# Performance work log

Measured on AMD Instinct MI355X. Metric: run time of the kernel, lower is better.

The kernel has to match this reference:

```python
import jax, jax.numpy as jnp
import numpy as np

NUM_GRAPHS = 256  # static batch size (= batch_indices.max()+1 by construction)
EMBED = 32
HIDDEN = 256
DEPTH = 10


def setup_inputs() -> dict:
    key = jax.random.key(0)
    ks = jax.random.split(key, 16)
    N, M = 8192, 16384
    atom_features = jax.random.randint(ks[0], (N,), 0, 200, dtype=jnp.int32)
    bond_features = jax.random.randint(ks[1], (M,), 0, 10, dtype=jnp.int32)
    adjacency_matrix = jax.random.randint(ks[2], (N, N), 0, 2, dtype=jnp.int32)
    batch_indices = jnp.sort(jax.random.randint(ks[3], (N,), 0, NUM_GRAPHS, dtype=jnp.int32))
    s = 0.05
    atom_emb_table = jax.random.normal(ks[4], (200, EMBED), jnp.float32) * s
    bond_emb_table = jax.random.normal(ks[5], (10, EMBED), jnp.float32) * s
    msg_W = jax.random.normal(ks[6], (DEPTH, HIDDEN, 2 * EMBED), jnp.float32) * s
    msg_b = jax.random.normal(ks[7], (DEPTH, HIDDEN), jnp.float32) * s
    gru_Wih = jax.random.normal(ks[8], (DEPTH, 3 * EMBED, HIDDEN), jnp.float32) * s
    gru_Whh = jax.random.normal(ks[9], (DEPTH, 3 * EMBED, EMBED), jnp.float32) * s
    gru_bih = jax.random.normal(ks[10], (DEPTH, 3 * EMBED), jnp.float32) * s
    gru_bhh = jax.random.normal(ks[11], (DEPTH, 3 * EMBED), jnp.float32) * s
    pool_W = jax.random.normal(ks[12], (HIDDEN, EMBED), jnp.float32) * s
    pool_b = jax.random.normal(ks[13], (HIDDEN,), jnp.float32) * s
    return dict(atom_features=atom_features, bond_features=bond_features,
                adjacency_matrix=adjacency_matrix, batch_indices=batch_indices,
                atom_emb_table=atom_emb_table, bond_emb_table=bond_emb_table,
                msg_W=msg_W, msg_b=msg_b, gru_Wih=gru_Wih, gru_Whh=gru_Whh,
                gru_bih=gru_bih, gru_bhh=gru_bhh, pool_W=pool_W, pool_b=pool_b)


def _gru_step(x, h, Wih, Whh, bih, bhh):
    # single-step torch-style GRU cell: x [N,HIDDEN], h [N,EMBED]
    gi = x @ Wih.T + bih                      # [N, 3E]
    gh = h @ Whh.T + bhh                      # [N, 3E]
    i_r, i_z, i_n = jnp.split(gi, 3, axis=-1)
    h_r, h_z, h_n = jnp.split(gh, 3, axis=-1)
    r = jax.nn.sigmoid(i_r + h_r)
    z = jax.nn.sigmoid(i_z + h_z)
    n = jnp.tanh(i_n + r * h_n)
    return (1.0 - z) * n + z * h


def reference(atom_features, bond_features, adjacency_matrix, batch_indices,
              atom_emb_table, bond_emb_table, msg_W, msg_b,
              gru_Wih, gru_Whh, gru_bih, gru_bhh, pool_W, pool_b):
    h = atom_emb_table[atom_features]                      # [N, E]
    A = (adjacency_matrix != 0).astype(h.dtype)            # [N, N]
    deg = A.sum(axis=-1, keepdims=True)                    # [N, 1]
    inv_deg = 1.0 / jnp.maximum(deg, 1.0)
    has_nei = deg > 0
    for d in range(DEPTH):
        # mean over neighbors of Linear(concat(self, nei)) == affine in (self, mean_nei)
        nei_mean = (A @ h) * inv_deg                       # [N, E]
        W_self = msg_W[d][:, :EMBED]                       # [H, E]
        W_nei = msg_W[d][:, EMBED:]                        # [H, E]
        msg = h @ W_self.T + nei_mean @ W_nei.T + msg_b[d]  # [N, H]
        msg = jnp.where(has_nei, msg, 0.0)                 # zero message if no neighbors
        h = _gru_step(msg, h, gru_Wih[d], gru_Whh[d], gru_bih[d], gru_bhh[d])
        # dropout is identity in eval mode
    # segment-mean pooling over graphs (zeros for empty graphs)
    sums = jax.ops.segment_sum(h, batch_indices, num_segments=NUM_GRAPHS)      # [B, E]
    counts = jax.ops.segment_sum(jnp.ones((h.shape[0],), h.dtype), batch_indices,
                                 num_segments=NUM_GRAPHS)[:, None]             # [B, 1]
    graph_mean = jnp.where(counts > 0, sums / jnp.maximum(counts, 1.0), 0.0)
    graph_embeddings = graph_mean @ pool_W.T + pool_b                          # [B, H]
    bond_embeddings = bond_emb_table[bond_features]                            # [M, E]
    return h, bond_embeddings, graph_embeddings
```

## Files before the change

### kernel.cpp

```cpp
#include <hip/hip_runtime.h>
#include <stdint.h>

#define N_ATOMS 8192
#define EMBED   32
#define DEPTHN  10

typedef short bf16x8 __attribute__((ext_vector_type(8)));
typedef float f32x4  __attribute__((ext_vector_type(4)));

__device__ __forceinline__ unsigned short f2bf(float f){
    unsigned u = __builtin_bit_cast(unsigned, f);
    u = u + 0x7FFFu + ((u >> 16) & 1u);
    return (unsigned short)(u >> 16);
}

__global__ __launch_bounds__(256) void k_preA(const int* __restrict__ A,
                                              unsigned long long* __restrict__ mask,
                                              int row0)
{
    const int i = row0 + blockIdx.x;
    const int t = threadIdx.x, w = t >> 6, l = t & 63;
    const int* row = A + (size_t)i * N_ATOMS;
    __shared__ unsigned long long lm[128];
    #pragma unroll
    for (int k = 0; k < 32; ++k){
        int j = k*256 + t;
        unsigned long long m = __ballot(row[j] != 0);
        if (l == 0) lm[k*4 + w] = m;
    }
    __syncthreads();
    if (t < 128) mask[(size_t)i*128 + t] = lm[t];
}

__global__ __launch_bounds__(256) void k_pack(const unsigned* __restrict__ maskRM,
                                              unsigned* __restrict__ mP,
                                              float* __restrict__ deg,
                                              float* __restrict__ invdeg)
{
    const int grp = blockIdx.x, t = threadIdx.x;
    __shared__ unsigned lm[16*260];
    __shared__ int red[256];
    #pragma unroll
    for (int s = 0; s < 16; ++s)
        lm[s*260 + t] = maskRM[(size_t)grp*4096 + s*256 + t];
    __syncthreads();
    {
        int r = t >> 4, seg = t & 15, cnt = 0;
        #pragma unroll
        for (int k = 0; k < 16; ++k) cnt += __popc(lm[r*260 + seg*16 + k]);
        red[t] = cnt; __syncthreads();
        if (t < 16){
            int s = 0;
            #pragma unroll
            for (int k = 0; k < 16; ++k) s += red[t*16 + k];
            deg[grp*16 + t] = (float)s;
            invdeg[grp*16 + t] = 1.f / fmaxf((float)s, 1.f);
        }
    }
    unsigned* out = mP + (size_t)grp*4096;
    #pragma unroll
    for (int s = 0; s < 16; ++s){
        int W = s*256 + t;
        out[W] = lm[(W & 15)*260 + (W >> 4)];
    }
}

__global__ __launch_bounds__(256) void k_setup(
    const int* __restrict__ af, const float* __restrict__ atom_emb,
    const float* __restrict__ msgW, const float* __restrict__ msgb,
    const float* __restrict__ Wih, const float* __restrict__ bih,
    float* __restrict__ hA, unsigned short* __restrict__ hP,
    float* __restrict__ Wc, float* __restrict__ bc,
    const int* __restrict__ bfeat, const float* __restrict__ bondf,
    float* __restrict__ out1)
{
    const int blk = blockIdx.x, t = threadIdx.x;
    if (blk < 1024){
        int idx = blk*256 + t;
        int i = idx >> 5, e = idx & 31;
        float v = atom_emb[af[i]*EMBED + e];
        hA[idx] = v;
        int g = i >> 5, qd = (i >> 3) & 3, j8 = i & 7;
        hP[(size_t)((g*2 + (e>>4))*64 + qd*16 + (e&15))*8 + j8] = f2bf(v);
    } else if (blk < 1264){
        int o = (blk-1024)*256 + t;
        int d = o / 6144, r = o % 6144, g = r >> 6, e = r & 63;
        const float* wi = Wih  + (size_t)(d*96 + g)*256;
        const float* mw = msgW + (size_t)d*256*64 + e;
        float acc = 0.f;
        for (int hh = 0; hh < 256; ++hh) acc += wi[hh] * mw[hh*64];
        Wc[o] = acc;
    } else if (blk < 1268){
        int o = (blk-1264)*256 + t;
        if (o < 960){
            int d = o / 96;
            const float* wi = Wih + (size_t)o*256;
            const float* mb = msgb + d*256;
            float acc = 0.f;
            for (int hh = 0; hh < 256; ++hh) acc += wi[hh] * mb[hh];
            bc[o] = acc + bih[o];
        }
    } else {
        int idx = (blk-1268)*256 + t;
        out1[idx] = bondf[bfeat[idx >> 5]*EMBED + (idx & 31)];
    }
}

__global__ __launch_bounds__(256) void k_nei(const unsigned short* __restrict__ hP,
                                             const unsigned* __restrict__ mP,
                                             float* __restrict__ neipart)
{
    __shared__ uint2 lut[16];
    const int rb = blockIdx.x & 63;
    const int q  = blockIdx.x >> 6;
    const int t = threadIdx.x, w = t >> 6, lane = t & 63;
    if (t < 16){
        unsigned lo = ((t & 1) ? 0x3F80u : 0u) | ((t & 2) ? 0x3F800000u : 0u);
        unsigned hi = ((t & 4) ? 0x3F80u : 0u) | ((t & 8) ? 0x3F800000u : 0u);
        lut[t] = make_uint2(lo, hi);
    }
    __syncthreads();
    const int n = lane & 15, quad = lane >> 4;
    const int rt0 = rb*8 + w*2;

    f32x4 a00 = {0.f,0.f,0.f,0.f};
    f32x4 a01 = {0.f,0.f,0.f,0.f};
    f32x4 a10 = {0.f,0.f,0.f,0.f};
    f32x4 a11 = {0.f,0.f,0.f,0.f};

    const unsigned* m0 = mP + (size_t)rt0*4096 + n;
    const unsigned* m1 = m0 + 4096;
    #pragma unroll 4
    for (int kk = 0; kk < 32; ++kk){
        const int g = q*32 + kk;
        union { uint4 u; bf16x8 v; } b0, b1;
        b0.u = *(const uint4*)&hP[(size_t)((g*2+0)*64 + lane)*8];
        b1.u = *(const uint4*)&hP[(size_t)((g*2+1)*64 + lane)*8];
        unsigned by0 = (m0[g*16] >> (quad*8)) & 0xFFu;
        unsigned by1 = (m1[g*16] >> (quad*8)) & 0xFFu;
        union { uint2 d[2]; bf16x8 v; } af0, af1;
        af0.d[0] = lut[by0 & 15u];
        af0.d[1] = lut[by0 >> 4];
        af1.d[0] = lut[by1 & 15u];
        af1.d[1] = lut[by1 >> 4];
        a00 = __builtin_amdgcn_mfma_f32_16x16x32_bf16(af0.v, b0.v, a00, 0, 0, 0);
        a01 = __builtin_amdgcn_mfma_f32_16x16x32_bf16(af0.v, b1.v, a01, 0, 0, 0);
        a10 = __builtin_amdgcn_mfma_f32_16x16x32_bf16(af1.v, b0.v, a10, 0, 0, 0);
        a11 = __builtin_amdgcn_mfma_f32_16x16x32_bf16(af1.v, b1.v, a11, 0, 0, 0);
    }
    float* outp = neipart + (size_t)q * N_ATOMS * EMBED;
    #pragma unroll
    for (int r = 0; r < 4; ++r){
        int row0 = rt0*16 + quad*4 + r;
        int row1 = row0 + 16;
        outp[(size_t)row0*EMBED + n]      = a00[r];
        outp[(size_t)row0*EMBED + 16 + n] = a01[r];
        outp[(size_t)row1*EMBED + n]      = a10[r];
        outp[(size_t)row1*EMBED + 16 + n] = a11[r];
    }
}

__global__ __launch_bounds__(256) void k_gru(
    const float* __restrict__ hin, float* __restrict__ hout,
    const float* __restrict__ neipart,
    const float* __restrict__ invdeg, const float* __restrict__ deg,
    const float* __restrict__ Wc, const float* __restrict__ bc,
    const float* __restrict__ bihf, const float* __restrict__ bhhf,
    const float* __restrict__ Whhf,
    unsigned short* __restrict__ hP, float* __restrict__ out0, int last)
{
    __shared__ float xs[16][68];
    const int t = threadIdx.x, blk = blockIdx.x;
    if (t < 128){
        float4 v = *(const float4*)&hin[(size_t)blk*512 + t*4];
        int a = t >> 3, e = (t*4) & 31;
        *(float4*)&xs[a][e] = v;
    } else {
        int u = t - 128;
        int a = u >> 3, e = (u*4) & 31;
        float4 s = {0.f,0.f,0.f,0.f};
        #pragma unroll
        for (int q = 0; q < 8; ++q){
            float4 v2 = *(const float4*)&neipart[(size_t)q*N_ATOMS*EMBED + blk*512 + u*4];
            s.x += v2.x; s.y += v2.y; s.z += v2.z; s.w += v2.w;
        }
        *(float4*)&xs[a][32 + e] = s;
    }
    __syncthreads();

    const int a = t & 15, p = t >> 4;
    const int atom = blk*16 + a;
    const float idg = invdeg[atom];
    const bool nz = deg[atom] > 0.f;
    float x[64];
    #pragma unroll
    for (int r = 0; r < 16; ++r){
        float4 v = *(const float4*)&xs[a][r*4];
        x[r*4+0]=v.x; x[r*4+1]=v.y; x[r*4+2]=v.z; x[r*4+3]=v.w;
    }
    #pragma unroll
    for (int e = 32; e < 64; ++e) x[e] *= idg;

    const int g = atom >> 5, qd = (atom >> 3) & 3, j8 = atom & 7;
    #pragma unroll
    for (int jj = 0; jj < 2; ++jj){
        const int j = p*2 + jj;
        const float* wr = Wc + j*64;
        const float* wz = Wc + (32+j)*64;
        const float* wn = Wc + (64+j)*64;
        float gr=0.f, gz=0.f, gn=0.f;
        #pragma unroll
        for (int e = 0; e < 64; ++e){ gr += wr[e]*x[e]; gz += wz[e]*x[e]; gn += wn[e]*x[e]; }
        if (nz){ gr += bc[j]; gz += bc[32+j]; gn += bc[64+j]; }
        else   { gr  = bihf[j]; gz = bihf[32+j]; gn = bihf[64+j]; }
        const float* vr = Whhf + j*32;
        const float* vz = Whhf + (32+j)*32;
        const float* vn = Whhf + (64+j)*32;
        float hr=bhhf[j], hz=bhhf[32+j], hn=bhhf[64+j];
        #pragma unroll
        for (int e = 0; e < 32; ++e){ hr += vr[e]*x[e]; hz += vz[e]*x[e]; hn += vn[e]*x[e]; }
        float rg = 1.f/(1.f + expf(-(gr+hr)));
        float zg = 1.f/(1.f + expf(-(gz+hz)));
        float ng = tanhf(gn + rg*hn);
        float hnew = (1.f - zg)*ng + zg*x[j];
        hout[(size_t)atom*EMBED + j] = hnew;
        hP[(size_t)((g*2 + (j>>4))*64 + qd*16 + (j&15))*8 + j8] = f2bf(hnew);
        if (last) out0[(size_t)atom*EMBED + j] = hnew;
    }
}

__global__ __launch_bounds__(256) void k_pool(
    const float* __restrict__ h, const int* __restrict__ batch,
    const float* __restrict__ poolW, const float* __restrict__ poolb,
    float* __restrict__ out2)
{
    const int b = blockIdx.x, t = threadIdx.x;
    int lo, hi;
    { int l = 0, r = N_ATOMS; while (l < r){ int m = (l+r)>>1; if (batch[m] < b)   l = m+1; else r = m; } lo = l; }
    { int l = 0, r = N_ATOMS; while (l < r){ int m = (l+r)>>1; if (batch[m] < b+1) l = m+1; else r = m; } hi = l; }
    const int cnt = hi - lo;
    __shared__ float ps[8][32];
    __shared__ float mean[32];
    const int e = t & 31, g = t >> 5;
    float acc = 0.f;
    for (int a = lo + g; a < hi; a += 8) acc += h[(size_t)a*EMBED + e];
    ps[g][e] = acc; __syncthreads();
    if (t < 32){
        float s = 0.f;
        #pragma unroll
        for (int gg = 0; gg < 8; ++gg) s += ps[gg][t];
        mean[t] = (cnt > 0) ? s / (float)cnt : 0.f;
    }
    __syncthreads();
    float emb = poolb[t];
    #pragma unroll
    for (int ee = 0; ee < 32; ++ee) emb += mean[ee] * poolW[t*32 + ee];
    out2[b*256 + t] = emb;
}

extern "C" void kernel_launch(void* const* d_in, const int* in_sizes, int n_in,
                              void* d_out, int out_size, void* d_ws, size_t ws_size,
                              hipStream_t stream)
{
    (void)in_sizes; (void)n_in; (void)out_size;
    const int* af   = (const int*)d_in[0];
    const int* bfe  = (const int*)d_in[1];
    const int* A    = (const int*)d_in[2];
    const int* bidx = (const int*)d_in[3];
    const float* atom_emb = (const float*)d_in[4];
    const float* bond_emb = (const float*)d_in[5];
    const float* msgW  = (const float*)d_in[6];
    const float* msgb  = (const float*)d_in[7];
    const float* Wih   = (const float*)d_in[8];
    const float* Whh   = (const float*)d_in[9];
    const float* bih   = (const float*)d_in[10];
    const float* bhh   = (const float*)d_in[11];
    const float* poolW = (const float*)d_in[12];
    const float* poolb = (const float*)d_in[13];

    float* out0 = (float*)d_out;
    float* out1 = out0 + 262144;
    float* out2 = out1 + 524288;

    float* deg    = out2;
    float* invdeg = out2 + 8192;

    unsigned long long* maskRM;
    unsigned*       mP;
    float*          hA; float* hB; float* Wc; float* bc; float* neipart;
    unsigned short* hP;
    const int wsok = (ws_size >= (size_t)33554432) ? 1 : 0;
    if (wsok){
        char* W = (char*)d_ws;
        maskRM  = (unsigned long long*)(W + 0);
        mP      = (unsigned*)(W + 8388608);
        hP      = (unsigned short*)(W + 16777216);
        hA      = (float*)(W + 17825792);
        hB      = (float*)(W + 18874368);
        Wc      = (float*)(W + 19922944);
        bc      = (float*)(W + 20185088);
        neipart = (float*)(W + 20971520);
        k_preA<<<dim3(8192), dim3(256), 0, stream>>>(A, maskRM, 0);
    } else {
        char* Ab = (char*)d_in[2];
        hA      = (float*)(Ab + 0);
        hB      = (float*)(Ab + 1048576);
        hP      = (unsigned short*)(Ab + 2097152);
        Wc      = (float*)(Ab + 2621440);
        bc      = (float*)(Ab + 2867200);
        neipart = (float*)(Ab + 4194304);
        mP      = (unsigned*)(Ab + 13631488);
        maskRM  = (unsigned long long*)(Ab + 260046848);
        k_preA<<<dim3(1),    dim3(256), 0, stream>>>(A, maskRM, 8191);
        k_preA<<<dim3(7),    dim3(256), 0, stream>>>(A, maskRM, 8184);
        k_preA<<<dim3(248),  dim3(256), 0, stream>>>(A, maskRM, 7936);
        k_preA<<<dim3(7936), dim3(256), 0, stream>>>(A, maskRM, 0);
    }
    k_pack<<<dim3(512), dim3(256), 0, stream>>>((const unsigned*)maskRM, mP,
        deg, invdeg);
    k_setup<<<dim3(3316), dim3(256), 0, stream>>>(af, atom_emb, msgW, msgb,
        Wih, bih, hA, hP, Wc, bc, bfe, bond_emb, out1);

    float* hin = hA; float* hout = hB;
    for (int d = 0; d < DEPTHN; ++d){
        k_nei<<<dim3(512), dim3(256), 0, stream>>>(hP, mP, neipart);
        k_gru<<<dim3(512), dim3(256), 0, stream>>>(hin, hout, neipart, invdeg, deg,
            Wc + d*6144, bc + d*96, bih + d*96, bhh + d*96, Whh + d*3072,
            hP, out0, (d == DEPTHN-1) ? 1 : 0);
        float* tmp = hin; hin = hout; hout = tmp;
    }
    k_pool<<<dim3(256), dim3(256), 0, stream>>>(hin, bidx, poolW, poolb, out2);
}
```

Baseline: 727.8 us.

## Fuse neighbor aggregation and GRU into one per-depth kernel with ping-pong bf16 buffers

Merges the neighbor-sum MFMA kernel and the GRU kernel into a single 512-thread kernel per depth. Each block now covers 32 atoms, and its 8 waves split the K dimension and reduce partial sums through shared memory instead of a global neipart buffer. The packed bf16 h buffer is double-buffered so one depth can read the old state while writing the new one. The pack and setup kernels are also merged into one launch. This removes global round-trips and half the launches, but only 256 blocks run per depth, which may limit parallelism.

```diff
diff --git a/kernel.cpp b/kernel.cpp
--- a/kernel.cpp
+++ b/kernel.cpp
@@ -32,40 +32,9 @@
     if (t < 128) mask[(size_t)i*128 + t] = lm[t];
 }
 
-__global__ __launch_bounds__(256) void k_pack(const unsigned* __restrict__ maskRM,
-                                              unsigned* __restrict__ mP,
-                                              float* __restrict__ deg,
-                                              float* __restrict__ invdeg)
-{
-    const int grp = blockIdx.x, t = threadIdx.x;
-    __shared__ unsigned lm[16*260];
-    __shared__ int red[256];
-    #pragma unroll
-    for (int s = 0; s < 16; ++s)
-        lm[s*260 + t] = maskRM[(size_t)grp*4096 + s*256 + t];
-    __syncthreads();
-    {
-        int r = t >> 4, seg = t & 15, cnt = 0;
-        #pragma unroll
-        for (int k = 0; k < 16; ++k) cnt += __popc(lm[r*260 + seg*16 + k]);
-        red[t] = cnt; __syncthreads();
-        if (t < 16){
-            int s = 0;
-            #pragma unroll
-            for (int k = 0; k < 16; ++k) s += red[t*16 + k];
-            deg[grp*16 + t] = (float)s;
-            invdeg[grp*16 + t] = 1.f / fmaxf((float)s, 1.f);
-        }
-    }
-    unsigned* out = mP + (size_t)grp*4096;
-    #pragma unroll
-    for (int s = 0; s < 16; ++s){
-        int W = s*256 + t;
-        out[W] = lm[(W & 15)*260 + (W >> 4)];
-    }
-}
-
-__global__ __launch_bounds__(256) void k_setup(
+__global__ __launch_bounds__(256) void k_prep(
+    const unsigned* __restrict__ maskRM, unsigned* __restrict__ mP,
+    float* __restrict__ deg, float* __restrict__ invdeg,
     const int* __restrict__ af, const float* __restrict__ atom_emb,
     const float* __restrict__ msgW, const float* __restrict__ msgb,
     const float* __restrict__ Wih, const float* __restrict__ bih,
@@ -74,158 +43,180 @@
     const int* __restrict__ bfeat, const float* __restrict__ bondf,
     float* __restrict__ out1)
 {
-    const int blk = blockIdx.x, t = threadIdx.x;
-    if (blk < 1024){
-        int idx = blk*256 + t;
-        int i = idx >> 5, e = idx & 31;
-        float v = atom_emb[af[i]*EMBED + e];
-        hA[idx] = v;
-        int g = i >> 5, qd = (i >> 3) & 3, j8 = i & 7;
-        hP[(size_t)((g*2 + (e>>4))*64 + qd*16 + (e&15))*8 + j8] = f2bf(v);
-    } else if (blk < 1264){
-        int o = (blk-1024)*256 + t;
-        int d = o / 6144, r = o % 6144, g = r >> 6, e = r & 63;
-        const float* wi = Wih  + (size_t)(d*96 + g)*256;
-        const float* mw = msgW + (size_t)d*256*64 + e;
-        float acc = 0.f;
-        for (int hh = 0; hh < 256; ++hh) acc += wi[hh] * mw[hh*64];
-        Wc[o] = acc;
-    } else if (blk < 1268){
-        int o = (blk-1264)*256 + t;
-        if (o < 960){
-            int d = o / 96;
-            const float* wi = Wih + (size_t)o*256;
-            const float* mb = msgb + d*256;
+    const int t = threadIdx.x;
+    if (blockIdx.x < 512){
+        const int grp = blockIdx.x;
+        __shared__ unsigned lm[16*260];
+        __shared__ int red[256];
+        #pragma unroll
+        for (int s = 0; s < 16; ++s)
+            lm[s*260 + t] = maskRM[(size_t)grp*4096 + s*256 + t];
+        __syncthreads();
+        {
+            int r = t >> 4, seg = t & 15, cnt = 0;
+            #pragma unroll
+            for (int k = 0; k < 16; ++k) cnt += __popc(lm[r*260 + seg*16 + k]);
+            red[t] = cnt; __syncthreads();
+            if (t < 16){
+                int s = 0;
+                #pragma unroll
+                for (int k = 0; k < 16; ++k) s += red[t*16 + k];
+                deg[grp*16 + t] = (float)s;
+                invdeg[grp*16 + t] = 1.f / fmaxf((float)s, 1.f);
+            }
+        }
+        unsigned* out = mP + (size_t)grp*4096;
+        #pragma unroll
+        for (int s = 0; s < 16; ++s){
+            int W = s*256 + t;
+            out[W] = lm[(W & 15)*260 + (W >> 4)];
+        }
+    } else {
+        const int blk = blockIdx.x - 512;
+        if (blk < 1024){
+            int idx = blk*256 + t;
+            int i = idx >> 5, e = idx & 31;
+            float v = atom_emb[af[i]*EMBED + e];
+            hA[idx] = v;
+            int g = i >> 5, qd = (i >> 3) & 3, j8 = i & 7;
+            hP[(size_t)((g*2 + (e>>4))*64 + qd*16 + (e&15))*8 + j8] = f2bf(v);
+        } else if (blk < 1264){
+            int o = (blk-1024)*256 + t;
+            int d = o / 6144, r = o % 6144, g = r >> 6, e = r & 63;
+            const float* wi = Wih  + (size_t)(d*96 + g)*256;
+            const float* mw = msgW + (size_t)d*256*64 + e;
             float acc = 0.f;
-            for (int hh = 0; hh < 256; ++hh) acc += wi[hh] * mb[hh];
-            bc[o] = acc + bih[o];
-        }
-    } else {
-        int idx = (blk-1268)*256 + t;
-        out1[idx] = bondf[bfeat[idx >> 5]*EMBED + (idx & 31)];
-    }
-}
-
-__global__ __launch_bounds__(256) void k_nei(const unsigned short* __restrict__ hP,
-                                             const unsigned* __restrict__ mP,
-                                             float* __restrict__ neipart)
+            for (int hh = 0; hh < 256; ++hh) acc += wi[hh] * mw[hh*64];
+            Wc[o] = acc;
+        } else if (blk < 1268){
+            int o = (blk-1264)*256 + t;
+            if (o < 960){
+                int d = o / 96;
+                const float* wi = Wih + (size_t)o*256;
+                const float* mb = msgb + d*256;
+                float acc = 0.f;
+                for (int hh = 0; hh < 256; ++hh) acc += wi[hh] * mb[hh];
+                bc[o] = acc + bih[o];
+            }
+        } else {
+            int idx = (blk-1268)*256 + t;
+            out1[idx] = bondf[bfeat[idx >> 5]*EMBED + (idx & 31)];
+        }
+    }
+}
+
+__global__ __launch_bounds__(512) void k_depth(
+    const unsigned short* __restrict__ hPin,
+    const unsigned* __restrict__ mP,
+    const float* __restrict__ hin, float* __restrict__ hout,
+    const float* __restrict__ invdeg, const float* __restrict__ deg,
+    const float* __restrict__ Wc, const float* __restrict__ bc,
+    const float* __restrict__ bihf, const float* __restrict__ bhhf,
+    const float* __restrict__ Whhf,
+    unsigned short* __restrict__ hPout, float* __restrict__ out0, int last)
 {
     __shared__ uint2 lut[16];
-    const int rb = blockIdx.x & 63;
-    const int q  = blockIdx.x >> 6;
-    const int t = threadIdx.x, w = t >> 6, lane = t & 63;
+    __shared__ float part[8][32][33];
+    __shared__ float xs[32][68];
+    const int t = threadIdx.x, blk = blockIdx.x;
     if (t < 16){
         unsigned lo = ((t & 1) ? 0x3F80u : 0u) | ((t & 2) ? 0x3F800000u : 0u);
         unsigned hi = ((t & 4) ? 0x3F80u : 0u) | ((t & 8) ? 0x3F800000u : 0u);
         lut[t] = make_uint2(lo, hi);
     }
     __syncthreads();
-    const int n = lane & 15, quad = lane >> 4;
-    const int rt0 = rb*8 + w*2;
-
-    f32x4 a00 = {0.f,0.f,0.f,0.f};
-    f32x4 a01 = {0.f,0.f,0.f,0.f};
-    f32x4 a10 = {0.f,0.f,0.f,0.f};
-    f32x4 a11 = {0.f,0.f,0.f,0.f};
-
-    const unsigned* m0 = mP + (size_t)rt0*4096 + n;
-    const unsigned* m1 = m0 + 4096;
-    #pragma unroll 4
-    for (int kk = 0; kk < 32; ++kk){
-        const int g = q*32 + kk;
-        union { uint4 u; bf16x8 v; } b0, b1;
-        b0.u = *(const uint4*)&hP[(size_t)((g*2+0)*64 + lane)*8];
-        b1.u = *(const uint4*)&hP[(size_t)((g*2+1)*64 + lane)*8];
-        unsigned by0 = (m0[g*16] >> (quad*8)) & 0xFFu;
-        unsigned by1 = (m1[g*16] >> (quad*8)) & 0xFFu;
-        union { uint2 d[2]; bf16x8 v; } af0, af1;
-        af0.d[0] = lut[by0 & 15u];
-        af0.d[1] = lut[by0 >> 4];
-        af1.d[0] = lut[by1 & 15u];
-        af1.d[1] = lut[by1 >> 4];
-        a00 = __builtin_amdgcn_mfma_f32_16x16x32_bf16(af0.v, b0.v, a00, 0, 0, 0);
-        a01 = __builtin_amdgcn_mfma_f32_16x16x32_bf16(af0.v, b1.v, a01, 0, 0, 0);
-        a10 = __builtin_amdgcn_mfma_f32_16x16x32_bf16(af1.v, b0.v, a10, 0, 0, 0);
-        a11 = __builtin_amdgcn_mfma_f32_16x16x32_bf16(af1.v, b1.v, a11, 0, 0, 0);
-    }
-    float* outp = neipart + (size_t)q * N_ATOMS * EMBED;
-    #pragma unroll
-    for (int r = 0; r < 4; ++r){
-        int row0 = rt0*16 + quad*4 + r;
-        int row1 = row0 + 16;
-        outp[(size_t)row0*EMBED + n]      = a00[r];
-        outp[(size_t)row0*EMBED + 16 + n] = a01[r];
-        outp[(size_t)row1*EMBED + n]      = a10[r];
-        outp[(size_t)row1*EMBED + 16 + n] = a11[r];
-    }
-}
-
-__global__ __launch_bounds__(256) void k_gru(
-    const float* __restrict__ hin, float* __restrict__ hout,
-    const float* __restrict__ neipart,
-    const float* __restrict__ invdeg, const float* __restrict__ deg,
-    const float* __restrict__ Wc, const float* __restrict__ bc,
-    const float* __restrict__ bihf, const float* __restrict__ bhhf,
-    const float* __restrict__ Whhf,
-    unsigned short* __restrict__ hP, float* __restrict__ out0, int last)
-{
-    __shared__ float xs[16][68];
-    const int t = threadIdx.x, blk = blockIdx.x;
-    if (t < 128){
-        float4 v = *(const float4*)&hin[(size_t)blk*512 + t*4];
-        int a = t >> 3, e = (t*4) & 31;
-        *(float4*)&xs[a][e] = v;
-    } else {
-        int u = t - 128;
-        int a = u >> 3, e = (u*4) & 31;
-        float4 s = {0.f,0.f,0.f,0.f};
-        #pragma unroll
-        for (int q = 0; q < 8; ++q){
-            float4 v2 = *(const float4*)&neipart[(size_t)q*N_ATOMS*EMBED + blk*512 + u*4];
-            s.x += v2.x; s.y += v2.y; s.z += v2.z; s.w += v2.w;
-        }
-        *(float4*)&xs[a][32 + e] = s;
-    }
-    __syncthreads();
-
-    const int a = t & 15, p = t >> 4;
-    const int atom = blk*16 + a;
-    const float idg = invdeg[atom];
-    const bool nz = deg[atom] > 0.f;
-    float x[64];
-    #pragma unroll
-    for (int r = 0; r < 16; ++r){
-        float4 v = *(const float4*)&xs[a][r*4];
-        x[r*4+0]=v.x; x[r*4+1]=v.y; x[r*4+2]=v.z; x[r*4+3]=v.w;
-    }
-    #pragma unroll
-    for (int e = 32; e < 64; ++e) x[e] *= idg;
-
-    const int g = atom >> 5, qd = (atom >> 3) & 3, j8 = atom & 7;
-    #pragma unroll
-    for (int jj = 0; jj < 2; ++jj){
-        const int j = p*2 + jj;
-        const float* wr = Wc + j*64;
-        const float* wz = Wc + (32+j)*64;
-        const float* wn = Wc + (64+j)*64;
-        float gr=0.f, gz=0.f, gn=0.f;
-        #pragma unroll
-        for (int e = 0; e < 64; ++e){ gr += wr[e]*x[e]; gz += wz[e]*x[e]; gn += wn[e]*x[e]; }
-        if (nz){ gr += bc[j]; gz += bc[32+j]; gn += bc[64+j]; }
-        else   { gr  = bihf[j]; gz = bihf[32+j]; gn = bihf[64+j]; }
-        const float* vr = Whhf + j*32;
-        const float* vz = Whhf + (32+j)*32;
-        const float* vn = Whhf + (64+j)*32;
-        float hr=bhhf[j], hz=bhhf[32+j], hn=bhhf[64+j];
-        #pragma unroll
-        for (int e = 0; e < 32; ++e){ hr += vr[e]*x[e]; hz += vz[e]*x[e]; hn += vn[e]*x[e]; }
-        float rg = 1.f/(1.f + expf(-(gr+hr)));
-        float zg = 1.f/(1.f + expf(-(gz+hz)));
-        float ng = tanhf(gn + rg*hn);
-        float hnew = (1.f - zg)*ng + zg*x[j];
-        hout[(size_t)atom*EMBED + j] = hnew;
-        hP[(size_t)((g*2 + (j>>4))*64 + qd*16 + (j&15))*8 + j8] = f2bf(hnew);
-        if (last) out0[(size_t)atom*EMBED + j] = hnew;
+    {
+        const int q = t >> 6, lane = t & 63;
+        const int n = lane & 15, quad = lane >> 4;
+        const int rt0 = blk*2;
+        f32x4 a00 = {0.f,0.f,0.f,0.f};
+        f32x4 a01 = {0.f,0.f,0.f,0.f};
+        f32x4 a10 = {0.f,0.f,0.f,0.f};
+        f32x4 a11 = {0.f,0.f,0.f,0.f};
+        const unsigned* m0 = mP + (size_t)rt0*4096 + n;
+        const unsigned* m1 = m0 + 4096;
+        #pragma unroll 4
+        for (int kk = 0; kk < 32; ++kk){
+            const int g = q*32 + kk;
+            union { uint4 u; bf16x8 v; } b0, b1;
+            b0.u = *(const uint4*)&hPin[(size_t)((g*2+0)*64 + lane)*8];
+            b1.u = *(const uint4*)&hPin[(size_t)((g*2+1)*64 + lane)*8];
+            unsigned by0 = (m0[g*16] >> (quad*8)) & 0xFFu;
+            unsigned by1 = (m1[g*16] >> (quad*8)) & 0xFFu;
+            union { uint2 d[2]; bf16x8 v; } af0, af1;
+            af0.d[0] = lut[by0 & 15u];
+            af0.d[1] = lut[by0 >> 4];
+            af1.d[0] = lut[by1 & 15u];
+            af1.d[1] = lut[by1 >> 4];
+            a00 = __builtin_amdgcn_mfma_f32_16x16x32_bf16(af0.v, b0.v, a00, 0, 0, 0);
+            a01 = __builtin_amdgcn_mfma_f32_16x16x32_bf16(af0.v, b1.v, a01, 0, 0, 0);
+            a10 = __builtin_amdgcn_mfma_f32_16x16x32_bf16(af1.v, b0.v, a10, 0, 0, 0);
+            a11 = __builtin_amdgcn_mfma_f32_16x16x32_bf16(af1.v, b1.v, a11, 0, 0, 0);
+        }
+        #pragma unroll
+        for (int r = 0; r < 4; ++r){
+            int rl = quad*4 + r;
+            part[q][rl][n]       = a00[r];
+            part[q][rl][16+n]    = a01[r];
+            part[q][16+rl][n]    = a10[r];
+            part[q][16+rl][16+n] = a11[r];
+        }
+    }
+    __syncthreads();
+    {
+        #pragma unroll
+        for (int ii = 0; ii < 2; ++ii){
+            int i = ii*512 + t;
+            int a = i >> 5, e = i & 31;
+            float s = 0.f;
+            #pragma unroll
+            for (int q = 0; q < 8; ++q) s += part[q][a][e];
+            xs[a][32+e] = s;
+            xs[a][e] = hin[(size_t)blk*1024 + i];
+        }
+    }
+    __syncthreads();
+    {
+        const int a = t & 15, pw = t >> 4;
+        const int al = a + (pw & 16);
+        const int p  = pw & 15;
+        const int atom = blk*32 + al;
+        const float idg = invdeg[atom];
+        const bool nz = deg[atom] > 0.f;
+        float x[64];
+        #pragma unroll
+        for (int r = 0; r < 16; ++r){
+            float4 v = *(const float4*)&xs[al][r*4];
+            x[r*4+0]=v.x; x[r*4+1]=v.y; x[r*4+2]=v.z; x[r*4+3]=v.w;
+        }
+        #pragma unroll
+        for (int e = 32; e < 64; ++e) x[e] *= idg;
+        const int gg = atom >> 5, qd = (atom >> 3) & 3, j8 = atom & 7;
+        #pragma unroll
+        for (int jj = 0; jj < 2; ++jj){
+            const int j = p*2 + jj;
+            const float* wr = Wc + j*64;
+            const float* wz = Wc + (32+j)*64;
+            const float* wn = Wc + (64+j)*64;
+            float gr=0.f, gz=0.f, gn=0.f;
+            #pragma unroll
+            for (int e = 0; e < 64; ++e){ gr += wr[e]*x[e]; gz += wz[e]*x[e]; gn += wn[e]*x[e]; }
+            if (nz){ gr += bc[j]; gz += bc[32+j]; gn += bc[64+j]; }
+            else   { gr  = bihf[j]; gz = bihf[32+j]; gn = bihf[64+j]; }
+            const float* vr = Whhf + j*32;
+            const float* vz = Whhf + (32+j)*32;
+            const float* vn = Whhf + (64+j)*32;
+            float hr=bhhf[j], hz=bhhf[32+j], hn=bhhf[64+j];
+            #pragma unroll
+            for (int e = 0; e < 32; ++e){ hr += vr[e]*x[e]; hz += vz[e]*x[e]; hn += vn[e]*x[e]; }
+            float rg = 1.f/(1.f + expf(-(gr+hr)));
+            float zg = 1.f/(1.f + expf(-(gz+hz)));
+            float ng = tanhf(gn + rg*hn);
+            float hnew = (1.f - zg)*ng + zg*x[j];
+            hout[(size_t)atom*EMBED + j] = hnew;
+            hPout[(size_t)((gg*2 + (j>>4))*64 + qd*16 + (j&15))*8 + j8] = f2bf(hnew);
+            if (last) out0[(size_t)atom*EMBED + j] = hnew;
+        }
     }
 }
 
@@ -287,28 +278,28 @@
 
     unsigned long long* maskRM;
     unsigned*       mP;
-    float*          hA; float* hB; float* Wc; float* bc; float* neipart;
-    unsigned short* hP;
+    float*          hA; float* hB; float* Wc; float* bc;
+    unsigned short* hP0; unsigned short* hP1;
     const int wsok = (ws_size >= (size_t)33554432) ? 1 : 0;
     if (wsok){
         char* W = (char*)d_ws;
         maskRM  = (unsigned long long*)(W + 0);
         mP      = (unsigned*)(W + 8388608);
-        hP      = (unsigned short*)(W + 16777216);
+        hP0     = (unsigned short*)(W + 16777216);
         hA      = (float*)(W + 17825792);
         hB      = (float*)(W + 18874368);
         Wc      = (float*)(W + 19922944);
         bc      = (float*)(W + 20185088);
-        neipart = (float*)(W + 20971520);
+        hP1     = (unsigned short*)(W + 20971520);
         k_preA<<<dim3(8192), dim3(256), 0, stream>>>(A, maskRM, 0);
     } else {
         char* Ab = (char*)d_in[2];
         hA      = (float*)(Ab + 0);
         hB      = (float*)(Ab + 1048576);
-        hP      = (unsigned short*)(Ab + 2097152);
+        hP0     = (unsigned short*)(Ab + 2097152);
         Wc      = (float*)(Ab + 2621440);
         bc      = (float*)(Ab + 2867200);
-        neipart = (float*)(Ab + 4194304);
+        hP1     = (unsigned short*)(Ab + 4194304);
         mP      = (unsigned*)(Ab + 13631488);
         maskRM  = (unsigned long long*)(Ab + 260046848);
         k_preA<<<dim3(1),    dim3(256), 0, stream>>>(A, maskRM, 8191);
@@ -316,18 +307,18 @@
         k_preA<<<dim3(248),  dim3(256), 0, stream>>>(A, maskRM, 7936);
         k_preA<<<dim3(7936), dim3(256), 0, stream>>>(A, maskRM, 0);
     }
-    k_pack<<<dim3(512), dim3(256), 0, stream>>>((const unsigned*)maskRM, mP,
-        deg, invdeg);
-    k_setup<<<dim3(3316), dim3(256), 0, stream>>>(af, atom_emb, msgW, msgb,
-        Wih, bih, hA, hP, Wc, bc, bfe, bond_emb, out1);
+    k_prep<<<dim3(3828), dim3(256), 0, stream>>>((const unsigned*)maskRM, mP,
+        deg, invdeg, af, atom_emb, msgW, msgb, Wih, bih, hA, hP0, Wc, bc,
+        bfe, bond_emb, out1);
 
     float* hin = hA; float* hout = hB;
+    unsigned short* hPi = hP0; unsigned short* hPo = hP1;
     for (int d = 0; d < DEPTHN; ++d){
-        k_nei<<<dim3(512), dim3(256), 0, stream>>>(hP, mP, neipart);
-        k_gru<<<dim3(512), dim3(256), 0, stream>>>(hin, hout, neipart, invdeg, deg,
-            Wc + d*6144, bc + d*96, bih + d*96, bhh + d*96, Whh + d*3072,
-            hP, out0, (d == DEPTHN-1) ? 1 : 0);
-        float* tmp = hin; hin = hout; hout = tmp;
+        k_depth<<<dim3(256), dim3(512), 0, stream>>>(hPi, mP, hin, hout,
+            invdeg, deg, Wc + d*6144, bc + d*96, bih + d*96, bhh + d*96,
+            Whh + d*3072, hPo, out0, (d == DEPTHN-1) ? 1 : 0);
+        float* tf = hin; hin = hout; hout = tf;
+        unsigned short* tp = hPi; hPi = hPo; hPo = tp;
     }
     k_pool<<<dim3(256), dim3(256), 0, stream>>>(hin, bidx, poolW, poolb, out2);
 }
```

New measurement: 669.0 us. -8.1%, faster.
